# Optimization experiments

Hardware: AMD Instinct MI355X
Metric: run time of the kernel (lower is better)

## Reference

```python
import jax, jax.numpy as jnp
import numpy as np

N_HEAD = 8
HEAD_DIM = 64
DIM = 512
INNER = N_HEAD * HEAD_DIM
ATT_THRESHOLD = 1e-4
SCALE = HEAD_DIM ** -0.5


def setup_inputs() -> dict:
    key = jax.random.key(0)
    ks = jax.random.split(key, 7)
    b, n, dn = 2, 2048, 2048
    fr = jax.random.normal(ks[0], (b, n, DIM), dtype=jnp.float32)
    dt = jax.random.normal(ks[1], (b, dn, DIM), dtype=jnp.float32)
    s = DIM ** -0.5
    Wq = jax.random.normal(ks[2], (DIM, INNER), dtype=jnp.float32) * s
    Wk = jax.random.normal(ks[3], (DIM, INNER), dtype=jnp.float32) * s
    Wv = jax.random.normal(ks[4], (DIM, INNER), dtype=jnp.float32) * s
    Wo = jax.random.normal(ks[5], (INNER, DIM), dtype=jnp.float32) * (INNER ** -0.5)
    bo = jax.random.normal(ks[6], (DIM,), dtype=jnp.float32) * 0.01
    return {"fr": fr, "dt": dt, "Wq": Wq, "Wk": Wk, "Wv": Wv, "Wo": Wo, "bo": bo}


def reference(fr, dt, Wq, Wk, Wv, Wo, bo):
    b, n, _ = fr.shape
    dn = dt.shape[1]
    # projections -> [b, seq, n_head, head_dim]
    q = (fr @ Wq).reshape(b, n, N_HEAD, HEAD_DIM)
    k = (dt @ Wk).reshape(b, dn, N_HEAD, HEAD_DIM)
    v = (dt @ Wv).reshape(b, dn, N_HEAD, HEAD_DIM)
    # full attention matrix [b, h, n, dn]
    scores = jnp.einsum('bihd,bjhd->bhij', q, k) * SCALE
    attn = jax.nn.softmax(scores, axis=-1)
    # torch .clip(t) with one positional arg clamps the MIN: max(attn, t)
    attn = jnp.maximum(attn, ATT_THRESHOLD) - ATT_THRESHOLD
    attn = attn / jnp.sum(attn, axis=-1, keepdims=True)
    out = jnp.einsum('bhij,bjhd->bihd', attn, v).reshape(b, n, INNER)
    return out @ Wo + bo
```

## Files before the change

### kernel.cpp

```cpp
#include <hip/hip_runtime.h>
#include <hip/hip_bf16.h>

#define BB 2
#define SEQ 2048
#define NHEAD 8
#define HD 64
#define ATT_T 1e-4f
#define QSCALE 0.18033688011112042f

typedef short s16x8 __attribute__((ext_vector_type(8)));
typedef float f32x16 __attribute__((ext_vector_type(16)));

#define MFMA32(a, b, c) __builtin_amdgcn_mfma_f32_32x32x16_bf16((a), (b), (c), 0, 0, 0)
#define EXP2(x) __builtin_amdgcn_exp2f(x)
#define SB0() __builtin_amdgcn_sched_barrier(0)
#define WAITVM0() __builtin_amdgcn_s_waitcnt(0x0F70)
#define WAITVM4() __builtin_amdgcn_s_waitcnt(0x0F74)
#define WAITVM8() __builtin_amdgcn_s_waitcnt(0x0F78)

__device__ __forceinline__ unsigned short bfr(float x) {
  __hip_bfloat16 h = __float2bfloat16(x);
  return __builtin_bit_cast(unsigned short, h);
}
__device__ __forceinline__ unsigned int packbf(float a, float b) {
  return (unsigned int)bfr(a) | ((unsigned int)bfr(b) << 16);
}
__device__ __forceinline__ unsigned int permpack(float a, float b) {
  return __builtin_amdgcn_perm(__builtin_bit_cast(unsigned int, b),
                               __builtin_bit_cast(unsigned int, a), 0x07060302u);
}
__device__ __forceinline__ void async16(const void* g, void* l) {
  __builtin_amdgcn_global_load_lds(
      (const __attribute__((address_space(1))) unsigned int*)g,
      (__attribute__((address_space(3))) unsigned int*)l, 16, 0, 0);
}
__device__ __forceinline__ void plswap(unsigned a, unsigned b, int lh,
                                       unsigned& x, unsigned& z) {
#if __has_builtin(__builtin_amdgcn_permlane32_swap)
  typedef unsigned uint2v __attribute__((ext_vector_type(2)));
  uint2v r = __builtin_amdgcn_permlane32_swap(a, b, false, false);
  x = r[0];
  z = r[1];
#else
  unsigned ea = (unsigned)__shfl_xor((int)a, 32);
  unsigned eb = (unsigned)__shfl_xor((int)b, 32);
  x = lh ? eb : a;
  z = lh ? b : ea;
#endif
}

__global__ __launch_bounds__(256) void prep(const float* __restrict__ fr,
                                            const float* __restrict__ dt,
                                            const float* __restrict__ w0,
                                            const float* __restrict__ w1,
                                            const float* __restrict__ w2,
                                            const float* __restrict__ w3,
                                            unsigned short* __restrict__ frB,
                                            unsigned short* __restrict__ dtB,
                                            unsigned short* __restrict__ o0,
                                            unsigned short* __restrict__ o1,
                                            unsigned short* __restrict__ o2,
                                            unsigned short* __restrict__ o3) {
  const int bid = blockIdx.x;
  if (bid < 2048) {
    const float* src = (bid < 1024) ? fr : dt;
    unsigned short* dst = (bid < 1024) ? frB : dtB;
    const int chunk = (bid < 1024) ? bid : bid - 1024;
    const size_t base = (size_t)chunk * 2048 + threadIdx.x * 8;
    float4 a = *(const float4*)(src + base);
    float4 b = *(const float4*)(src + base + 4);
    uint4 o;
    o.x = packbf(a.x, a.y);
    o.y = packbf(a.z, a.w);
    o.z = packbf(b.x, b.y);
    o.w = packbf(b.z, b.w);
    *(uint4*)(dst + base) = o;
    return;
  }
  __shared__ float tle[64][65];
  const int t = bid - 2048;
  const int z = t >> 6, by = (t >> 3) & 7, bx = t & 7;
  const float* W = z == 0 ? w0 : z == 1 ? w1 : z == 2 ? w2 : w3;
  unsigned short* WT = z == 0 ? o0 : z == 1 ? o1 : z == 2 ? o2 : o3;
  const int r0 = by * 64, c0 = bx * 64;
  const int tr = threadIdx.x >> 4;
  const int tc = threadIdx.x & 15;
  #pragma unroll
  for (int i = 0; i < 4; i++) {
    int r = tr + i * 16;
    float4 v = *(const float4*)(W + (size_t)(r0 + r) * 512 + c0 + tc * 4);
    tle[r][tc * 4 + 0] = v.x;
    tle[r][tc * 4 + 1] = v.y;
    tle[r][tc * 4 + 2] = v.z;
    tle[r][tc * 4 + 3] = v.w;
  }
  __syncthreads();
  #pragma unroll
  for (int i = 0; i < 4; i++) {
    int c = tr + i * 16;
    int rr = tc * 4;
    uint2 p;
    p.x = packbf(tle[rr + 0][c], tle[rr + 1][c]);
    p.y = packbf(tle[rr + 2][c], tle[rr + 3][c]);
    *(uint2*)(WT + (size_t)(c0 + c) * 512 + r0 + rr) = p;
  }
}

__global__ __launch_bounds__(256) void gemm_qkv(const unsigned short* __restrict__ frB,
                                                const unsigned short* __restrict__ dtB,
                                                const unsigned short* __restrict__ WqT,
                                                const unsigned short* __restrict__ WkT,
                                                const unsigned short* __restrict__ WvT,
                                                unsigned short* __restrict__ Qp,
                                                unsigned short* __restrict__ Kp,
                                                unsigned short* __restrict__ VTp) {
  __shared__ __align__(16) unsigned short smem[24576];
  unsigned short* Asm = smem;
  unsigned short* Bsm = smem + 8192;
  const int tid = threadIdx.x, lane = tid & 63, w = tid >> 6;
  const int l31 = lane & 31, lh = lane >> 5;
  const int m0 = blockIdx.y * 64, n0 = blockIdx.x * 128;
  const int z = blockIdx.z;
  const unsigned short* Ab = z == 0 ? frB : dtB;
  const unsigned short* BT = z == 0 ? WqT : (z == 1 ? WkT : WvT);
  unsigned short* OP = z == 0 ? Qp : (z == 1 ? Kp : VTp);
  const float scale = z == 0 ? QSCALE : 1.0f;

  auto stage = [&](int kt, int buf) {
    const int k0 = kt * 64;
    #pragma unroll
    for (int i = 0; i < 2; i++) {
      int r = w * 2 + i, g = r >> 2, ks = r & 3;
      async16(Ab + (size_t)(m0 + g * 32 + l31) * 512 + k0 + ks * 16 + lh * 8,
              Asm + buf * 4096 + r * 512);
    }
    #pragma unroll
    for (int i = 0; i < 4; i++) {
      int r = w * 4 + i, gn = r >> 2, ks = r & 3;
      async16(BT + (size_t)(n0 + gn * 32 + l31) * 512 + k0 + ks * 16 + lh * 8,
              Bsm + buf * 8192 + r * 512);
    }
  };

  f32x16 acc[2];
  #pragma unroll
  for (int j = 0; j < 2; j++)
    #pragma unroll
    for (int r = 0; r < 16; r++) acc[j][r] = 0.f;

  stage(0, 0);
  for (int kt = 0; kt < 8; ++kt) {
    __syncthreads();
    if (kt + 1 < 8) stage(kt + 1, (kt + 1) & 1);
    const int buf = kt & 1;
    const unsigned short* as = Asm + buf * 4096 + (w & 1) * 2048;
    const unsigned short* bs = Bsm + buf * 8192 + (w >> 1) * 4096;
    #pragma unroll
    for (int ks = 0; ks < 4; ++ks) {
      s16x8 af = *(const s16x8*)(as + ks * 512 + lane * 8);
      s16x8 b0 = *(const s16x8*)(bs + ks * 512 + lane * 8);
      s16x8 b1 = *(const s16x8*)(bs + 2048 + ks * 512 + lane * 8);
      acc[0] = MFMA32(af, b0, acc[0]);
      acc[1] = MFMA32(af, b1, acc[1]);
    }
  }

  const int wm = (w & 1) * 32, wn = (w >> 1) * 64;
  const int bb = m0 >> 11, s0 = m0 & 2047;
  __syncthreads();
  if (z <= 1) {
    #pragma unroll
    for (int j = 0; j < 2; j++)
      #pragma unroll
      for (int r = 0; r < 16; r++) {
        int mm = wm + (r & 3) + 8 * (r >> 2) + 4 * lh;
        int nn = wn + j * 32 + l31;
        smem[mm * 136 + nn] = bfr(acc[j][r] * scale);
      }
    __syncthreads();
    #pragma unroll
    for (int it = 0; it < 4; ++it) {
      int c = tid + it * 256;
      int mm = c >> 4, seg = c & 15;
      uint4 vdat = *(const uint4*)(smem + mm * 136 + seg * 8);
      int n = n0 + seg * 8, h = n >> 6, d = n & 63;
      *(uint4*)(OP + ((size_t)((bb * NHEAD + h) * SEQ + s0 + mm)) * HD + d) = vdat;
    }
  } else {
    #pragma unroll
    for (int j = 0; j < 2; j++)
      #pragma unroll
      for (int r = 0; r < 16; r += 2) {
        int mm = wm + (r & 3) + 8 * (r >> 2) + 4 * lh;
        int nn = wn + j * 32 + l31;
        *(unsigned int*)(smem + nn * 72 + mm) = packbf(acc[j][r], acc[j][r + 1]);
      }
    __syncthreads();
    #pragma unroll
    for (int it = 0; it < 4; ++it) {
      int c = tid + it * 256;
      int nn = c >> 3, seg = c & 7;
      uint4 vdat = *(const uint4*)(smem + nn * 72 + seg * 8);
      int n = n0 + nn, h = n >> 6, d = n & 63;
      *(uint4*)(OP + ((size_t)((bb * NHEAD + h) * HD + d)) * SEQ + s0 + seg * 8) = vdat;
    }
  }
}

__global__ __launch_bounds__(256) void gemm_out(const unsigned short* __restrict__ A,
                                                const unsigned short* __restrict__ BT,
                                                const float* __restrict__ bias,
                                                float* __restrict__ O) {
  __shared__ __align__(16) unsigned short smem[16384];
  unsigned short* Asm = smem;
  unsigned short* Bsm = smem + 8192;
  const int tid = threadIdx.x, lane = tid & 63, w = tid >> 6;
  const int l31 = lane & 31, lh = lane >> 5;
  const int m0 = blockIdx.y * 64, n0 = blockIdx.x * 64;

  auto stage = [&](int kt, int buf) {
    const int k0 = kt * 64;
    #pragma unroll
    for (int i = 0; i < 2; i++) {
      int r = w * 2 + i, g = r >> 2, ks = r & 3;
      async16(A + (size_t)(m0 + g * 32 + l31) * 512 + k0 + ks * 16 + lh * 8,
              Asm + buf * 4096 + r * 512);
      async16(BT + (size_t)(n0 + g * 32 + l31) * 512 + k0 + ks * 16 + lh * 8,
              Bsm + buf * 4096 + r * 512);
    }
  };

  f32x16 acc;
  #pragma unroll
  for (int r = 0; r < 16; r++) acc[r] = 0.f;

  stage(0, 0);
  for (int kt = 0; kt < 8; ++kt) {
    __syncthreads();
    if (kt + 1 < 8) stage(kt + 1, (kt + 1) & 1);
    const int buf = kt & 1;
    const unsigned short* as = Asm + buf * 4096 + (w & 1) * 2048;
    const unsigned short* bs = Bsm + buf * 4096 + (w >> 1) * 2048;
    #pragma unroll
    for (int ks = 0; ks < 4; ++ks) {
      s16x8 af = *(const s16x8*)(as + ks * 512 + lane * 8);
      s16x8 bf = *(const s16x8*)(bs + ks * 512 + lane * 8);
      acc = MFMA32(af, bf, acc);
    }
  }

  const int wm = (w & 1) * 32, wn = (w >> 1) * 32;
  float bv = bias[n0 + wn + l31];
  #pragma unroll
  for (int r = 0; r < 16; r++) {
    int mm = wm + (r & 3) + 8 * (r >> 2) + 4 * lh;
    O[(size_t)(m0 + mm) * 512 + n0 + wn + l31] = acc[r] + bv;
  }
}

__global__ __launch_bounds__(256, 2) void attn_mfma(const unsigned short* __restrict__ Q,
                                                    const unsigned short* __restrict__ K,
                                                    const unsigned short* __restrict__ VT,
                                                    unsigned short* __restrict__ O) {
  __shared__ __align__(16) unsigned short arena[4][4096];
  __shared__ float larr[4][64];
  __shared__ float warr[4][64];

  const int tid = threadIdx.x;
  const int lane = tid & 63;
  const int w = tid >> 6;
  const int l31 = lane & 31, lh = lane >> 5;

  const int bid = blockIdx.x;
  const int g = bid & 7, j = bid >> 3;
  const int bh = g * 2 + (j >> 5);
  const int qt = j & 31;

  const unsigned short* Qh = Q + (size_t)bh * SEQ * HD;
  const unsigned short* Kh = K + (size_t)bh * SEQ * HD;
  const unsigned short* VTh = VT + (size_t)bh * HD * SEQ;

  s16x8 qf[2][4];
  #pragma unroll
  for (int q2 = 0; q2 < 2; q2++)
    #pragma unroll
    for (int t = 0; t < 4; t++)
      qf[q2][t] = *(const s16x8*)(Qh + (size_t)(qt * 64 + q2 * 32 + l31) * HD + 16 * t + 8 * lh);

  unsigned short* kbuf = &arena[w][0];
  const int kbase = w * 512;

  auto stageK = [&](int c, int slot) {
    const unsigned short* base = Kh + (size_t)(kbase + c * 32 + l31) * HD + lh * 8;
    #pragma unroll
    for (int tt = 0; tt < 4; tt++)
      async16(base + tt * 16, kbuf + slot * 2048 + tt * 512);
  };

  f32x16 scp[2];
  auto qkt = [&](int slot) {
    s16x8 kf[4];
    #pragma unroll
    for (int tt = 0; tt < 4; tt++)
      kf[tt] = *(const s16x8*)(kbuf + slot * 2048 + tt * 512 + lane * 8);
    #pragma unroll
    for (int q2 = 0; q2 < 2; q2++) {
      f32x16 sc;
      #pragma unroll
      for (int r = 0; r < 16; r++) sc[r] = 0.f;
      #pragma unroll
      for (int tt = 0; tt < 4; tt++) sc = MFMA32(kf[tt], qf[q2][tt], sc);
      scp[q2] = sc;
    }
  };

  float lsum[2] = {0.f, 0.f};
  auto accum_l = [&]() {
    #pragma unroll
    for (int q2 = 0; q2 < 2; q2++) {
      float s0 = 0.f, s1 = 0.f, s2 = 0.f, s3 = 0.f;
      #pragma unroll
      for (int r = 0; r < 4; r++) {
        s0 += EXP2(scp[q2][r]);
        s1 += EXP2(scp[q2][4 + r]);
        s2 += EXP2(scp[q2][8 + r]);
        s3 += EXP2(scp[q2][12 + r]);
      }
      lsum[q2] += (s0 + s1) + (s2 + s3);
    }
  };

  stageK(0, 0);
  for (int c = 0; c < 16; ++c) {
    const int slot = c & 1;
    if (c + 1 < 16) stageK(c + 1, slot ^ 1);
    if (c > 0) accum_l();
    if (c + 1 < 16) { WAITVM4(); } else { WAITVM0(); }
    SB0();
    qkt(slot);
  }
  accum_l();
  #pragma unroll
  for (int q2 = 0; q2 < 2; q2++) lsum[q2] += __shfl_xor(lsum[q2], 32);
  if (lh == 0) { larr[w][l31] = lsum[0]; larr[w][32 + l31] = lsum[1]; }
  __syncthreads();
  float tl[2];
  #pragma unroll
  for (int q2 = 0; q2 < 2; q2++)
    tl[q2] = ATT_T * (larr[0][q2 * 32 + l31] + larr[1][q2 * 32 + l31] +
                      larr[2][q2 * 32 + l31] + larr[3][q2 * 32 + l31]);

  f32x16 acc[2][2];
  #pragma unroll
  for (int q2 = 0; q2 < 2; q2++)
    #pragma unroll
    for (int dh = 0; dh < 2; dh++)
      #pragma unroll
      for (int r = 0; r < 16; r++) acc[q2][dh][r] = 0.f;
  float wacc[2] = {0.f, 0.f};
  s16x8 vrA[4], vrB[4];

  auto loadV = [&](int c, s16x8(&vr)[4]) {
    #pragma unroll
    for (int dh = 0; dh < 2; dh++)
      #pragma unroll
      for (int kc = 0; kc < 2; kc++)
        vr[dh * 2 + kc] = *(const s16x8*)(VTh + (size_t)(dh * 32 + l31) * SEQ +
                                          kbase + c * 32 + kc * 16 + lh * 8);
  };
  auto softmax_pv = [&](const s16x8(&vr)[4]) {
    s16x8 pf[2][2];
    #pragma unroll
    for (int q2 = 0; q2 < 2; q2++) {
      uint2 quads[4];
      #pragma unroll
      for (int gq = 0; gq < 4; gq++) {
        float u0 = fmaxf(EXP2(scp[q2][4 * gq + 0]) - tl[q2], 0.f);
        float u1 = fmaxf(EXP2(scp[q2][4 * gq + 1]) - tl[q2], 0.f);
        float u2 = fmaxf(EXP2(scp[q2][4 * gq + 2]) - tl[q2], 0.f);
        float u3 = fmaxf(EXP2(scp[q2][4 * gq + 3]) - tl[q2], 0.f);
        wacc[q2] += (u0 + u1) + (u2 + u3);
        quads[gq].x = permpack(u0, u1);
        quads[gq].y = permpack(u2, u3);
      }
      #pragma unroll
      for (int tp = 0; tp < 2; tp++) {
        unsigned x0, z0, x1, z1;
        plswap(quads[2 * tp].x, quads[2 * tp + 1].x, lh, x0, z0);
        plswap(quads[2 * tp].y, quads[2 * tp + 1].y, lh, x1, z1);
        uint4 fr;
        fr.x = x0; fr.y = x1; fr.z = z0; fr.w = z1;
        pf[q2][tp] = __builtin_bit_cast(s16x8, fr);
      }
    }
    #pragma unroll
    for (int q2 = 0; q2 < 2; q2++)
      #pragma unroll
      for (int dh = 0; dh < 2; dh++) {
        acc[q2][dh] = MFMA32(pf[q2][0], vr[dh * 2 + 0], acc[q2][dh]);
        acc[q2][dh] = MFMA32(pf[q2][1], vr[dh * 2 + 1], acc[q2][dh]);
      }
  };

  stageK(0, 0);
  loadV(0, vrA);
  for (int cc = 0; cc < 16; cc += 2) {
    if (cc > 0) softmax_pv(vrB);
    stageK(cc + 1, 1);
    loadV(cc + 1, vrB);
    WAITVM8();
    SB0();
    qkt(0);
    softmax_pv(vrA);
    if (cc + 2 < 16) {
      stageK(cc + 2, 0);
      loadV(cc + 2, vrA);
      WAITVM8();
    } else {
      WAITVM0();
    }
    SB0();
    qkt(1);
  }
  softmax_pv(vrB);

  #pragma unroll
  for (int q2 = 0; q2 < 2; q2++) wacc[q2] += __shfl_xor(wacc[q2], 32);
  if (lh == 0) { warr[w][l31] = wacc[0]; warr[w][32 + l31] = wacc[1]; }
  __syncthreads();

  float* plane0 = (float*)&arena[0][0];
  float* plane1 = (float*)&arena[2][0];

  if (w >= 2) {
    float* pl = (w == 2) ? plane0 : plane1;
    #pragma unroll
    for (int q2 = 0; q2 < 2; q2++)
      #pragma unroll
      for (int dh = 0; dh < 2; dh++)
        #pragma unroll
        for (int r = 0; r < 16; r++) {
          int ql = q2 * 32 + (r & 3) + 8 * (r >> 2) + 4 * lh;
          pl[ql * 64 + dh * 32 + l31] = acc[q2][dh][r];
        }
  }
  __syncthreads();
  if (w < 2) {
    float* pl = (w == 0) ? plane0 : plane1;
    #pragma unroll
    for (int q2 = 0; q2 < 2; q2++)
      #pragma unroll
      for (int dh = 0; dh < 2; dh++)
        #pragma unroll
        for (int r = 0; r < 16; r++) {
          int ql = q2 * 32 + (r & 3) + 8 * (r >> 2) + 4 * lh;
          acc[q2][dh][r] += pl[ql * 64 + dh * 32 + l31];
        }
  }
  __syncthreads();
  if (w == 1) {
    #pragma unroll
    for (int q2 = 0; q2 < 2; q2++)
      #pragma unroll
      for (int dh = 0; dh < 2; dh++)
        #pragma unroll
        for (int r = 0; r < 16; r++) {
          int ql = q2 * 32 + (r & 3) + 8 * (r >> 2) + 4 * lh;
          plane0[ql * 64 + dh * 32 + l31] = acc[q2][dh][r];
        }
  }
  __syncthreads();
  unsigned short* otile = &arena[2][0];
  if (w == 0) {
    #pragma unroll
    for (int q2 = 0; q2 < 2; q2++)
      #pragma unroll
      for (int dh = 0; dh < 2; dh++)
        #pragma unroll
        for (int r = 0; r < 16; r++) {
          int ql = q2 * 32 + (r & 3) + 8 * (r >> 2) + 4 * lh;
          float wt = warr[0][ql] + warr[1][ql] + warr[2][ql] + warr[3][ql];
          float v = (acc[q2][dh][r] + plane0[ql * 64 + dh * 32 + l31]) / wt;
          otile[ql * 64 + dh * 32 + l31] = bfr(v);
        }
  }
  __syncthreads();
  const int b = bh >> 3, h = bh & 7;
  #pragma unroll
  for (int it = 0; it < 2; ++it) {
    int c2 = tid + it * 256;
    int mm = c2 >> 3, seg = c2 & 7;
    uint4 vdat = *(const uint4*)(otile + mm * 64 + seg * 8);
    *(uint4*)(O + ((size_t)(b * SEQ + qt * 64 + mm)) * 512 + h * HD + seg * 8) = vdat;
  }
}

extern "C" void kernel_launch(void* const* d_in, const int* in_sizes, int n_in,
                              void* d_out, int out_size, void* d_ws, size_t ws_size,
                              hipStream_t stream) {
  const float* fr = (const float*)d_in[0];
  const float* dt = (const float*)d_in[1];
  const float* Wq = (const float*)d_in[2];
  const float* Wk = (const float*)d_in[3];
  const float* Wv = (const float*)d_in[4];
  const float* Wo = (const float*)d_in[5];
  const float* bo = (const float*)d_in[6];
  float* out = (float*)d_out;

  const size_t planeE = (size_t)BB * SEQ * 512;
  const size_t wE = 512 * 512;
  unsigned short* p = (unsigned short*)d_ws;
  unsigned short* WqT = p; p += wE;
  unsigned short* WkT = p; p += wE;
  unsigned short* WvT = p; p += wE;
  unsigned short* WoT = p; p += wE;
  unsigned short* Qp  = p; p += planeE;
  unsigned short* Kp  = p; p += planeE;
  unsigned short* VTp = p; p += planeE;
  unsigned short* aoB = p; p += planeE;

  unsigned short* frB = (unsigned short*)d_out;
  unsigned short* dtB = (unsigned short*)d_out + planeE;

  prep<<<2304, 256, 0, stream>>>(fr, dt, Wq, Wk, Wv, Wo, frB, dtB, WqT, WkT, WvT, WoT);

  gemm_qkv<<<dim3(4, 64, 3), 256, 0, stream>>>(frB, dtB, WqT, WkT, WvT, Qp, Kp, VTp);

  attn_mfma<<<BB * NHEAD * 32, 256, 0, stream>>>(Qp, Kp, VTp, aoB);

  gemm_out<<<dim3(8, 64), 256, 0, stream>>>(aoB, WoT, bo, out);
}
```

Before: 164.0 us.

## Deepen K staging pipeline from double to quad buffering in attention kernel

Grows the LDS arena so K tiles can sit in four slots, and keeps three K chunks in flight in both the row-sum pass and the softmax/PV pass. The vmcnt waits are retuned to match the new outstanding load counts, and plane1 for the epilogue reduction moves to arena[1] to fit the larger slot size. The aim is to hide global-load latency better. The cost is doubling the arena's shared memory, which may reduce occupancy below the 2 blocks per CU targeted by the launch bounds.

```diff
diff --git a/kernel.cpp b/kernel.cpp
--- a/kernel.cpp
+++ b/kernel.cpp
@@ -17,6 +17,7 @@
 #define WAITVM0() __builtin_amdgcn_s_waitcnt(0x0F70)
 #define WAITVM4() __builtin_amdgcn_s_waitcnt(0x0F74)
 #define WAITVM8() __builtin_amdgcn_s_waitcnt(0x0F78)
+#define WAITVM12() __builtin_amdgcn_s_waitcnt(0x0F7C)
 
 __device__ __forceinline__ unsigned short bfr(float x) {
   __hip_bfloat16 h = __float2bfloat16(x);
@@ -262,7 +263,7 @@
                                                     const unsigned short* __restrict__ K,
                                                     const unsigned short* __restrict__ VT,
                                                     unsigned short* __restrict__ O) {
-  __shared__ __align__(16) unsigned short arena[4][4096];
+  __shared__ __align__(16) unsigned short arena[4][8192];
   __shared__ float larr[4][64];
   __shared__ float warr[4][64];
 
@@ -331,13 +332,17 @@
   };
 
   stageK(0, 0);
+  stageK(1, 1);
+  stageK(2, 2);
   for (int c = 0; c < 16; ++c) {
-    const int slot = c & 1;
-    if (c + 1 < 16) stageK(c + 1, slot ^ 1);
+    if (c + 3 < 16) stageK(c + 3, (c + 3) & 3);
     if (c > 0) accum_l();
-    if (c + 1 < 16) { WAITVM4(); } else { WAITVM0(); }
+    if (c < 13) { WAITVM12(); }
+    else if (c == 13) { WAITVM8(); }
+    else if (c == 14) { WAITVM4(); }
+    else { WAITVM0(); }
     SB0();
-    qkt(slot);
+    qkt(c & 3);
   }
   accum_l();
   #pragma unroll
@@ -403,25 +408,32 @@
   };
 
   stageK(0, 0);
+  stageK(1, 1);
+  stageK(2, 2);
   loadV(0, vrA);
   for (int cc = 0; cc < 16; cc += 2) {
-    if (cc > 0) softmax_pv(vrB);
-    stageK(cc + 1, 1);
+    if (cc > 0) {
+      if (cc < 14) { WAITVM12(); } else { WAITVM8(); }
+      SB0();
+      softmax_pv(vrB);
+    }
     loadV(cc + 1, vrB);
-    WAITVM8();
+    if (cc + 3 < 16) stageK(cc + 3, (cc + 3) & 3);
+    if (cc == 0) { WAITVM12(); }
     SB0();
-    qkt(0);
+    qkt(cc & 3);
+    if (cc == 0) { WAITVM8(); }
+    else if (cc < 14) { WAITVM12(); }
+    else { WAITVM4(); }
+    SB0();
     softmax_pv(vrA);
-    if (cc + 2 < 16) {
-      stageK(cc + 2, 0);
-      loadV(cc + 2, vrA);
-      WAITVM8();
-    } else {
-      WAITVM0();
-    }
+    if (cc + 2 < 16) loadV(cc + 2, vrA);
+    if (cc + 4 < 16) stageK(cc + 4, (cc + 4) & 3);
     SB0();
-    qkt(1);
-  }
+    qkt((cc + 1) & 3);
+  }
+  WAITVM0();
+  SB0();
   softmax_pv(vrB);
 
   #pragma unroll
@@ -430,7 +442,7 @@
   __syncthreads();
 
   float* plane0 = (float*)&arena[0][0];
-  float* plane1 = (float*)&arena[2][0];
+  float* plane1 = (float*)&arena[1][0];
 
   if (w >= 2) {
     float* pl = (w == 2) ? plane0 : plane1;
```

Result: no change. 164.1 us (+0.1%).
